# Kernel optimization log

Hardware: AMD Instinct MI355X
Metric: run time of the kernel (lower is better)

The kernel has to match this reference:

```python
import jax, jax.numpy as jnp
import numpy as np

B, C, H, W = 16, 256, 32, 32
DIM = H * W  # LayerNorm/Linear dim == h*w per the rearrange in forward


def _conv1x1(x, w, b):
    # x: [b,c,h,w], w: [out,in] (1x1 kernel squeezed), b: [out]
    return jnp.einsum('bchw,oc->bohw', x, w) + b[None, :, None, None]


def _layernorm(x, g, b, eps=1e-5):
    mu = jnp.mean(x, axis=-1, keepdims=True)
    var = jnp.var(x, axis=-1, keepdims=True)
    return (x - mu) / jnp.sqrt(var + eps) * g + b


def setup_inputs() -> dict:
    key = jax.random.key(0)
    ks = jax.random.split(key, 12)
    n = jax.random.normal
    k_cdc = (2.0 / (2 * C)) ** 0.5   # kaiming_normal fan_in = 2C
    k_v = (2.0 / C) ** 0.5           # fan_in = C
    k_lin = (2.0 / DIM) ** 0.5       # fan_in = DIM
    return {
        'x_spa': n(ks[0], (B, C, H, W), jnp.float32),
        'x_freq': n(ks[1], (B, C, H, W), jnp.float32),
        'w_cdc': n(ks[2], (C, 2 * C), jnp.float32) * k_cdc,
        'b_cdc': jnp.zeros((C,), jnp.float32),
        'w_sv': n(ks[3], (C, C), jnp.float32) * k_v,
        'b_sv': jnp.zeros((C,), jnp.float32),
        'w_fv': n(ks[4], (C, C), jnp.float32) * k_v,
        'b_fv': jnp.zeros((C,), jnp.float32),
        'ln_w': jnp.ones((DIM,), jnp.float32),
        'ln_b': jnp.zeros((DIM,), jnp.float32),
        'w_qk': n(ks[5], (2 * DIM, DIM), jnp.float32) * k_lin,  # Linear(dim, 2*dim), no bias
        'w_spa': n(ks[6], (DIM, DIM), jnp.float32) * k_lin,
        'b_spa': jnp.zeros((DIM,), jnp.float32),
        'w_frq': n(ks[7], (DIM, DIM), jnp.float32) * k_lin,
        'b_frq': jnp.zeros((DIM,), jnp.float32),
    }


def reference(x_spa, x_freq, w_cdc, b_cdc, w_sv, b_sv, w_fv, b_fv,
              ln_w, ln_b, w_qk, w_spa, b_spa, w_frq, b_frq):
    b, c, h, w = x_spa.shape
    hw = h * w
    scale = hw ** (-0.5)
    v_spa = _conv1x1(x_spa, w_sv, b_sv).reshape(b, c, hw)
    v_freq = _conv1x1(x_freq, w_fv, b_fv).reshape(b, c, hw)
    x = _conv1x1(jnp.concatenate([x_spa, x_freq], axis=1), w_cdc, b_cdc).reshape(b, c, hw)
    x = _layernorm(x, ln_w, ln_b)
    qk = x @ w_qk.T                       # [b, c, 2*hw]
    q, k = jnp.split(qk, 2, axis=-1)      # each [b, c, hw]
    att = jnp.einsum('bcn,bcm->bnm', q, k) * scale   # q^T k over channels: [b, hw, hw]
    att_spa = jax.nn.softmax(att @ w_spa.T + b_spa, axis=-1)
    att_frq = jax.nn.softmax(att @ w_frq.T + b_frq, axis=-1)
    out_spa = x_spa + jnp.einsum('bcn,bnm->bcm', v_spa, att_spa).reshape(b, c, h, w)
    out_freq = x_freq + jnp.einsum('bcn,bnm->bcm', v_freq, att_frq).reshape(b, c, h, w)
    return out_spa, out_freq
```

## Files before the change

kernel.cpp:

```cpp
#include <hip/hip_runtime.h>
#include <hip/hip_bf16.h>

typedef __hip_bfloat16 bf16;
typedef __attribute__((ext_vector_type(8))) short bf16x8v;
typedef __attribute__((ext_vector_type(4))) float f32x4v;

__device__ __forceinline__ float bfbits2f(unsigned short h) {
    union { unsigned int u; float f; } v; v.u = ((unsigned int)h) << 16; return v.f;
}
__device__ __forceinline__ unsigned short f2bfbits(float f) {
    bf16 h = __float2bfloat16(f);
    unsigned short s;
    __builtin_memcpy(&s, &h, 2);
    return s;
}
__device__ __forceinline__ float load1_any(const void* p, long idx, bool f32) {
    if (f32) return ((const float*)p)[idx];
    return bfbits2f(((const unsigned short*)p)[idx]);
}
__device__ __forceinline__ float4 loadbf4(const bf16* p) {
    ushort4 u = *reinterpret_cast<const ushort4*>(p);
    return make_float4(bfbits2f(u.x), bfbits2f(u.y), bfbits2f(u.z), bfbits2f(u.w));
}
__device__ __forceinline__ void store_bf4(bf16* p, float a, float b, float c, float d) {
    ushort4 o;
    o.x = f2bfbits(a); o.y = f2bfbits(b); o.z = f2bfbits(c); o.w = f2bfbits(d);
    *reinterpret_cast<ushort4*>(p) = o;
}
__device__ __forceinline__ void gl16(const void* g, void* l) {
    __builtin_amdgcn_global_load_lds(
        (const __attribute__((address_space(1))) unsigned int*)g,
        (__attribute__((address_space(3))) unsigned int*)l, 16, 0, 0);
}

__global__ __launch_bounds__(1024)
void detect_kernel(const unsigned short* __restrict__ x, int* __restrict__ flag) {
    const int tid = threadIdx.x;
    int zc = 0, hc = 0;
    const uint4* xv = (const uint4*)x;
#pragma unroll
    for (int p = 0; p < 16; ++p) {
        uint4 v = xv[p * 1024 + tid];
        unsigned s0 = v.x & 0xFFFFu, s1 = v.y & 0xFFFFu;
        unsigned s2 = v.z & 0xFFFFu, s3 = v.w & 0xFFFFu;
        zc += (int)(s0 == 0) + (int)(s1 == 0) + (int)(s2 == 0) + (int)(s3 == 0);
        hc += (int)(((s0 >> 7) & 0xFFu) >= 0x90u) + (int)(((s1 >> 7) & 0xFFu) >= 0x90u)
            + (int)(((s2 >> 7) & 0xFFu) >= 0x90u) + (int)(((s3 >> 7) & 0xFFu) >= 0x90u);
    }
#pragma unroll
    for (int off = 32; off > 0; off >>= 1) {
        zc += __shfl_down(zc, off);
        hc += __shfl_down(hc, off);
    }
    __shared__ int rz[16], rh[16];
    if ((tid & 63) == 0) { rz[tid >> 6] = zc; rh[tid >> 6] = hc; }
    __syncthreads();
    if (tid == 0) {
        int Z = 0, H = 0;
#pragma unroll
        for (int i = 0; i < 16; ++i) { Z += rz[i]; H += rh[i]; }
        flag[0] = (Z > 60000 || H > 256) ? 1 : 0;
        flag[1] = 1;
    }
}

__global__ void diag_kernel(float* __restrict__ out, float val) {
    if (threadIdx.x == 0) out[0] = val;
}

__global__ __launch_bounds__(256)
void convert6_kernel(const void* __restrict__ s0, const void* __restrict__ s1,
                     const void* __restrict__ s2, const void* __restrict__ s3,
                     const void* __restrict__ s4, const void* __restrict__ s5,
                     bf16* __restrict__ dst, const int* __restrict__ dflag) {
    const bool f32 = (*dflag != 0);
    for (long i = (long)blockIdx.x * 256 + threadIdx.x; i < 4456448;
         i += (long)gridDim.x * 256) {
        const void* s; long o;
        if (i < 131072)       { s = s0; o = i; }
        else if (i < 196608)  { s = s1; o = i - 131072; }
        else if (i < 262144)  { s = s2; o = i - 196608; }
        else if (i < 2359296) { s = s3; o = i - 262144; }
        else if (i < 3407872) { s = s4; o = i - 2359296; }
        else                  { s = s5; o = i - 3407872; }
        dst[i] = __float2bfloat16(load1_any(s, o, f32));
    }
}

__global__ __launch_bounds__(256)
void xpose_w_kernel(const bf16* __restrict__ src, bf16* __restrict__ dst) {
    __shared__ float t[64][65];
    const int c0 = blockIdx.x * 64, r0 = blockIdx.y * 64;
    const int tid = threadIdx.x;
#pragma unroll
    for (int p = 0; p < 16; ++p) {
        int e = tid + p * 256; int r = e >> 6, c = e & 63;
        t[r][c] = __bfloat162float(src[(long)(r0 + r) * 1024 + c0 + c]);
    }
    __syncthreads();
#pragma unroll
    for (int p = 0; p < 16; ++p) {
        int e = tid + p * 256; int r = e >> 6, c = e & 63;
        dst[(long)(c0 + r) * 1024 + r0 + c] = __float2bfloat16(t[c][r]);
    }
}

__global__ __launch_bounds__(256)
void build_wleft_kernel(const bf16* __restrict__ w_cdc, const bf16* __restrict__ w_sv,
                        const bf16* __restrict__ w_fv, bf16* __restrict__ W) {
    int i = blockIdx.x * 256 + threadIdx.x;
    if (i >= 393216) return;
    int r = i >> 9, c = i & 511;
    float v = 0.f;
    if (r < 256) v = __bfloat162float(w_cdc[r * 512 + c]);
    else if (r < 512) { if (c < 256) v = __bfloat162float(w_sv[(r - 256) * 256 + c]); }
    else              { if (c >= 256) v = __bfloat162float(w_fv[(r - 512) * 256 + (c - 256)]); }
    W[i] = __float2bfloat16(v);
}

__global__ __launch_bounds__(256)
void build_bcat_kernel(const void* __restrict__ b0, const void* __restrict__ b1,
                       const void* __restrict__ b2, float* __restrict__ bc,
                       const int* __restrict__ dflag) {
    const bool f32 = (*dflag != 0);
    int i = blockIdx.x * 256 + threadIdx.x;
    if (i < 256)      bc[i] = load1_any(b0, i, f32);
    else if (i < 512) bc[i] = load1_any(b1, i - 256, f32);
    else if (i < 768) bc[i] = load1_any(b2, i - 512, f32);
}

__global__ __launch_bounds__(256)
void xpose_conv_kernel(const void* __restrict__ x1, const void* __restrict__ x2,
                       bf16* __restrict__ dst, int bofs, int zsplit,
                       const int* __restrict__ dflag) {
    const bool f32 = (*dflag != 0);
    __shared__ float t[64][65];
    const int ch0 = blockIdx.y * 64, n0 = blockIdx.x * 64, z = blockIdx.z;
    const bool hiz = (z >= zsplit);
    const int zl = hiz ? z - zsplit : z;
    const void* x = hiz ? x2 : x1;
    const long sb = (long)(zl + bofs) * 262144, db = (long)z * 262144;
    const int tid = threadIdx.x;
#pragma unroll
    for (int p = 0; p < 16; ++p) {
        int e = tid + p * 256; int sch = e >> 6, sn = e & 63;
        t[sch][sn] = load1_any(x, sb + (long)(ch0 + sch) * 1024 + n0 + sn, f32);
    }
    __syncthreads();
#pragma unroll
    for (int p = 0; p < 16; ++p) {
        int e = tid + p * 256; int dn = e >> 6, dch = e & 63;
        dst[db + (long)(n0 + dn) * 256 + ch0 + dch] = __float2bfloat16(t[dch][dn]);
    }
}

__global__ __launch_bounds__(256)
void smnorm_kernel(bf16* __restrict__ X, float* __restrict__ invS) {
    const int tid = threadIdx.x;
    const int cg = tid & 7;
    const int js = tid >> 3;
    const int n0 = blockIdx.x * 64;
    const long zb = (long)blockIdx.y * 1048576;
    unsigned short* Xp = (unsigned short*)X + zb + n0 + cg * 8;

    float m[8];
#pragma unroll
    for (int q = 0; q < 8; ++q) m[q] = -3.4e38f;
#pragma unroll 4
    for (int r = 0; r < 32; ++r) {
        bf16x8v u = *(const bf16x8v*)(Xp + (long)(js * 32 + r) * 1024);
#pragma unroll
        for (int q = 0; q < 8; ++q)
            m[q] = fmaxf(m[q], bfbits2f((unsigned short)u[q]));
    }
    __shared__ float sh[32][8][8];
    __shared__ float Mc[64];
#pragma unroll
    for (int q = 0; q < 8; ++q) sh[js][cg][q] = m[q];
    __syncthreads();
    if (tid < 64) {
        float mm = -3.4e38f;
#pragma unroll 8
        for (int s = 0; s < 32; ++s) mm = fmaxf(mm, sh[s][tid >> 3][tid & 7]);
        Mc[tid] = mm;
    }
    __syncthreads();
    float M8[8], s8[8];
#pragma unroll
    for (int q = 0; q < 8; ++q) { M8[q] = Mc[cg * 8 + q]; s8[q] = 0.f; }
#pragma unroll 4
    for (int r = 0; r < 32; ++r) {
        long off = (long)(js * 32 + r) * 1024;
        bf16x8v u = *(const bf16x8v*)(Xp + off);
        bf16x8v o;
#pragma unroll
        for (int q = 0; q < 8; ++q) {
            float e = __expf(bfbits2f((unsigned short)u[q]) - M8[q]);
            s8[q] += e;
            o[q] = (short)f2bfbits(e);
        }
        *(bf16x8v*)(Xp + off) = o;
    }
    __syncthreads();
#pragma unroll
    for (int q = 0; q < 8; ++q) sh[js][cg][q] = s8[q];
    __syncthreads();
    if (tid < 64) {
        float ss = 0.f;
#pragma unroll 8
        for (int s = 0; s < 32; ++s) ss += sh[s][tid >> 3][tid & 7];
        invS[(long)blockIdx.y * 1024 + n0 + tid] = 1.0f / ss;
    }
}

__global__ __launch_bounds__(256)
void vscale_kernel(bf16* __restrict__ vb, const float* __restrict__ invS, int gN) {
    long base = ((long)blockIdx.x * 256 + threadIdx.x) * 8;
    if (base >= (long)512 * gN) return;
    int r = (int)(base / gN);
    long zn = base - (long)r * gN;
    const float* is = invS + (long)(r >> 8) * gN + zn;
    bf16x8v u = *(bf16x8v*)(vb + base);
    bf16x8v o;
#pragma unroll
    for (int q = 0; q < 8; ++q)
        o[q] = (short)f2bfbits(bfbits2f((unsigned short)u[q]) * is[q]);
    *(bf16x8v*)(vb + base) = o;
}

template <int MI, int EPI>
__global__ __launch_bounds__(256)
void mfma_nt(const bf16* __restrict__ A1, const bf16* __restrict__ A2,
             long aB1, long aB2, int ldA1, int ldA2,
             const bf16* __restrict__ B1, const bf16* __restrict__ B2,
             long bB1, long bB2, int ldB1, int ldB2,
             int ksplit, long kOff2,
             void* __restrict__ out1, void* __restrict__ out2,
             long oB1, long oB2, int ldO1, int ldO2,
             int K, float scale,
             const void* __restrict__ bias1, const void* __restrict__ bias2,
             const void* __restrict__ res1, const void* __restrict__ res2,
             long rBatch, int bofs, int zsplit,
             const int* __restrict__ dflag) {
    constexpr int BM = MI * 32;
    __shared__ short As[3][BM * 32];
    __shared__ short Bs[3][4096];
    const int tid  = threadIdx.x;
    const int lane = tid & 63, wave = tid >> 6;
    const int quad = lane >> 4, lrow = lane & 15;
    const int wm = (wave >> 1) * (MI * 16), wn = (wave & 1) * 64;

    int bx = blockIdx.x, by = blockIdx.y, bz = blockIdx.z;
    {
        const int gx = gridDim.x, gy = gridDim.y;
        const int gxy = gx * gy;
        const int ntot = gxy * gridDim.z;
        if ((ntot & 7) == 0) {
            int flat = bx + gx * (by + gy * bz);
            int w = (flat & 7) * (ntot >> 3) + (flat >> 3);
            bz = w / gxy;
            int rem = w - bz * gxy;
            by = rem / gx;
            bx = rem - by * gx;
        }
    }
    const int z  = bz;
    const bool hiz = (z >= zsplit);
    const int zl = hiz ? z - zsplit : z;
    const int n0 = bx * 128, m0 = by * BM;
    const int ldA = hiz ? ldA2 : ldA1, ldB = hiz ? ldB2 : ldB1;
    const int ldO = hiz ? ldO2 : ldO1;
    const int srow = tid >> 2, sseg = tid & 3;
    const int sl = sseg ^ ((srow >> 1) & 3);
    const int xq = quad ^ ((lrow >> 1) & 3);

    const bf16* Ab = (hiz ? A2 : A1) + (long)zl * (hiz ? aB2 : aB1);
    const bf16* Bb = (hiz ? B2 : B1) + (long)zl * (hiz ? bB2 : bB1);

    auto stage = [&](int buf, int k0) {
        const bf16* asrc = Ab + (long)k0;
        const bf16* bsrc = Bb + ((k0 < ksplit) ? (long)k0 : (long)(k0 - ksplit) + kOff2);
#pragma unroll
        for (int p = 0; p < MI / 2; ++p)
            gl16(asrc + (long)(m0 + p * 64 + srow) * ldA + sl * 8,
                 &As[buf][p * 2048 + wave * 512]);
        gl16(bsrc + (long)(n0 + srow) * ldB + sl * 8, &Bs[buf][wave * 512]);
        gl16(bsrc + (long)(n0 + 64 + srow) * ldB + sl * 8, &Bs[buf][2048 + wave * 512]);
    };

    f32x4v acc[MI][4] = {};
    const int nt = K >> 5;
    stage(0, 0);
    if (nt > 1) stage(1, 32);

    int cur = 0;
    for (int t = 0; t < nt; ++t) {
        if (t + 1 < nt) {
            if constexpr (MI == 4) asm volatile("s_waitcnt vmcnt(4)" ::: "memory");
            else                   asm volatile("s_waitcnt vmcnt(3)" ::: "memory");
        } else {
            asm volatile("s_waitcnt vmcnt(0)" ::: "memory");
        }
        __builtin_amdgcn_s_barrier();
        __builtin_amdgcn_sched_barrier(0);
        bf16x8v bfr[4], afr[MI];
#pragma unroll
        for (int j = 0; j < 4; ++j)
            bfr[j] = *(const bf16x8v*)&Bs[cur][(wn + j * 16 + lrow) * 32 + xq * 8];
#pragma unroll
        for (int i = 0; i < MI; ++i)
            afr[i] = *(const bf16x8v*)&As[cur][(wm + i * 16 + lrow) * 32 + xq * 8];
        asm volatile("s_waitcnt lgkmcnt(0)" ::: "memory");
        __builtin_amdgcn_sched_barrier(0);
        if (t + 2 < nt) {
            int nb = cur + 2; if (nb >= 3) nb -= 3;
            stage(nb, (t + 2) << 5);
        }
        __builtin_amdgcn_s_setprio(1);
#pragma unroll
        for (int i = 0; i < MI; ++i)
#pragma unroll
            for (int j = 0; j < 4; ++j)
                acc[i][j] = __builtin_amdgcn_mfma_f32_16x16x32_bf16(afr[i], bfr[j], acc[i][j], 0, 0, 0);
        __builtin_amdgcn_s_setprio(0);
        cur = (cur == 2) ? 0 : cur + 1;
    }

    const bool f32 = (*dflag != 0);
    const void* bias = hiz ? bias2 : bias1;
    if (EPI != 3) {
        bf16* O = (bf16*)(hiz ? out2 : out1) + (long)zl * (hiz ? oB2 : oB1);
#pragma unroll
        for (int i = 0; i < MI; ++i) {
            int row0 = m0 + wm + i * 16 + quad * 4;
            float rb[4] = {0.f, 0.f, 0.f, 0.f};
            if (EPI == 1 || EPI == 2) {
#pragma unroll
                for (int r = 0; r < 4; ++r) rb[r] = load1_any(bias, row0 + r, f32);
            }
#pragma unroll
            for (int j = 0; j < 4; ++j) {
                int col = n0 + wn + j * 16 + lrow;
#pragma unroll
                for (int r = 0; r < 4; ++r) {
                    float vv = acc[i][j][r];
                    if (EPI == 1) vv += rb[r];
                    if (EPI == 2) vv = vv * scale + rb[r];
                    O[(long)(row0 + r) * ldO + col] = __float2bfloat16(vv);
                }
            }
        }
    } else {
        float* O = (float*)(hiz ? out2 : out1);
        const void* res = hiz ? res2 : res1;
        const long ob  = (long)(zl + bofs) * (hiz ? oB2 : oB1);
        const long rbb = (long)(zl + bofs) * rBatch;
#pragma unroll
        for (int i = 0; i < MI; ++i) {
            int row0 = m0 + wm + i * 16 + quad * 4;
#pragma unroll
            for (int j = 0; j < 4; ++j) {
                int col = n0 + wn + j * 16 + lrow;
#pragma unroll
                for (int r = 0; r < 4; ++r) {
                    float rv = load1_any(res, rbb + (long)(row0 + r) * ldO + col, f32);
                    O[ob + (long)(row0 + r) * ldO + col] = acc[i][j][r] + rv;
                }
            }
        }
    }
}

__global__ __launch_bounds__(256)
void layernorm_kernel(const bf16* __restrict__ src, bf16* __restrict__ dst,
                      const void* __restrict__ g, const void* __restrict__ beta,
                      int gN, const int* __restrict__ dflag) {
    const bool f32 = (*dflag != 0);
    const int zc = blockIdx.x;
    const int zz = zc >> 8, c = zc & 255;
    const bf16* p = src + (long)c * gN + (long)zz * 1024;
    bf16* q = dst + (long)zc * 1024;
    const int tid = threadIdx.x;
    float4 v = loadbf4(p + tid * 4);
    float s  = v.x + v.y + v.z + v.w;
    float ss = v.x * v.x + v.y * v.y + v.z * v.z + v.w * v.w;
#pragma unroll
    for (int off = 32; off > 0; off >>= 1) {
        s  += __shfl_down(s, off);
        ss += __shfl_down(ss, off);
    }
    __shared__ float sh[8];
    __shared__ float sh_mu, sh_rs;
    if ((tid & 63) == 0) { sh[tid >> 6] = s; sh[4 + (tid >> 6)] = ss; }
    __syncthreads();
    if (tid == 0) {
        float S  = sh[0] + sh[1] + sh[2] + sh[3];
        float SS = sh[4] + sh[5] + sh[6] + sh[7];
        float mu = S * (1.0f / 1024.0f);
        float var = SS * (1.0f / 1024.0f) - mu * mu;
        sh_mu = mu;
        sh_rs = rsqrtf(fmaxf(var, 0.0f) + 1e-5f);
    }
    __syncthreads();
    float mu = sh_mu, rs = sh_rs;
    float gx = load1_any(g, tid * 4 + 0, f32), gy = load1_any(g, tid * 4 + 1, f32);
    float gz = load1_any(g, tid * 4 + 2, f32), gw = load1_any(g, tid * 4 + 3, f32);
    float bx = load1_any(beta, tid * 4 + 0, f32), by = load1_any(beta, tid * 4 + 1, f32);
    float bz = load1_any(beta, tid * 4 + 2, f32), bw = load1_any(beta, tid * 4 + 3, f32);
    store_bf4(q + tid * 4,
              (v.x - mu) * rs * gx + bx, (v.y - mu) * rs * gy + by,
              (v.z - mu) * rs * gz + bz, (v.w - mu) * rs * gw + bw);
}

extern "C" void kernel_launch(void* const* d_in, const int* in_sizes, int n_in,
                              void* d_out, int out_size, void* d_ws, size_t ws_size,
                              hipStream_t stream) {
    const void* x_spa  = d_in[0];
    const void* x_freq = d_in[1];
    const void* w_cdc  = d_in[2];
    const void* b_cdc  = d_in[3];
    const void* w_sv   = d_in[4];
    const void* b_sv   = d_in[5];
    const void* w_fv   = d_in[6];
    const void* b_fv   = d_in[7];
    const void* ln_w   = d_in[8];
    const void* ln_b   = d_in[9];
    const void* w_qk   = d_in[10];
    const void* w_spa  = d_in[11];
    const void* b_spa  = d_in[12];
    const void* w_frq  = d_in[13];
    const void* b_frq  = d_in[14];
    float* out = (float*)d_out;

    const int B = 16, C = 256;
    const long XB = 262144;
    const long PB = 1048576;

    int*   dflag = (int*)d_ws;
    float* bcat  = (float*)((char*)d_ws + 1024);
    bf16*  wb    = (bf16*)((char*)d_ws + 4096);
    bf16* w_cdc_b = wb;
    bf16* w_sv_b  = w_cdc_b + 131072;
    bf16* w_fv_b  = w_sv_b  + 65536;
    bf16* w_qk_b  = w_fv_b  + 65536;
    bf16* w_spa_b = w_qk_b  + 2097152;
    bf16* w_frq_b = w_spa_b + 1048576;
    bf16* w_qk_hiT= w_frq_b + 1048576;
    bf16* W1f     = w_qk_hiT + 1048576;
    bf16* Wleft   = W1f + 1048576;
    bf16* pb      = Wleft + 393216;

    const size_t fixedB = 4096 + 6946816ull * 2;
    const size_t perB   = 8921088ull;
    size_t avail = (ws_size > fixedB) ? (ws_size - fixedB) : 0;
    long gmax = (long)(avail / perB);
    const bool wsOK = (gmax >= 1);
    int G = wsOK ? (int)(gmax > 16 ? 16 : gmax) : 1;

    bf16* xT    = pb;
    bf16* XV    = xT  + 2L * G * XB;
    bf16* xln2  = XV  + 3L * G * XB;
    bf16* qTT   = xln2 + (long)G * XB;
    bf16* attpT = qTT + 3L * G * XB;
    float* invS = (float*)(attpT + 2L * G * PB);

    dim3 blk(256);
    detect_kernel<<<dim3(1), dim3(1024), 0, stream>>>((const unsigned short*)x_spa, dflag);

    if (!wsOK) {
        float mb = (float)(ws_size >> 20);
        diag_kernel<<<dim3(1), dim3(64), 0, stream>>>(out, 1000.0f * (mb + 1.0f));
        return;
    }

    convert6_kernel<<<dim3(4352), blk, 0, stream>>>(w_cdc, w_sv, w_fv, w_qk, w_spa, w_frq,
                                                    wb, dflag);
    xpose_w_kernel<<<dim3(16, 16), blk, 0, stream>>>(w_qk_b + 1048576, w_qk_hiT);
    build_wleft_kernel<<<dim3(1536), blk, 0, stream>>>(w_cdc_b, w_sv_b, w_fv_b, Wleft);
    build_bcat_kernel<<<dim3(3), blk, 0, stream>>>(b_cdc, b_sv, b_fv, bcat, dflag);
    mfma_nt<4, 0><<<dim3(8, 8, 2), blk, 0, stream>>>(
        w_spa_b, w_frq_b, 0, 0, 1024, 1024,
        w_qk_hiT, w_qk_hiT, 0, 0, 1024, 1024, 1024, 0,
        w_qk_b + 1048576, W1f, 0, 0, 1024, 1024,
        1024, 1.0f, nullptr, nullptr, nullptr, nullptr, 0, 0, 1, dflag);

    for (int b0 = 0; b0 < B; b0 += G) {
        int g = (B - b0 < G) ? (B - b0) : G;
        const int gN = g * 1024;
        bf16* vb = XV + 256L * gN;

        xpose_conv_kernel<<<dim3(16, 4, 2 * g), blk, 0, stream>>>(
            x_spa, x_freq, xT, b0, g, dflag);

        mfma_nt<4, 1><<<dim3(8 * g, 6, 1), blk, 0, stream>>>(
            Wleft, Wleft, 0, 0, 512, 512,
            xT, xT, 0, 0, 256, 256, 256, (long)g * XB,
            XV, XV, 0, 0, gN, gN,
            512, 1.0f, bcat, bcat, nullptr, nullptr, 0, 0, 1, dflag + 1);

        layernorm_kernel<<<dim3(g * C), blk, 0, stream>>>(XV, xln2, ln_w, ln_b, gN, dflag);

        mfma_nt<4, 0><<<dim3(2 * g, 8, 3), blk, 0, stream>>>(
            w_qk_b, W1f, 1048576, 0, 1024, 1024,
            xln2, xln2, 0, 0, 1024, 1024, 1024, 0,
            qTT, qTT + 2L * g * XB, (long)g * XB, 0, g * 256, g * 256,
            1024, 1.0f, nullptr, nullptr, nullptr, nullptr, 0, 0, 2, dflag);

        mfma_nt<4, 2><<<dim3(8, 8, 2 * g), blk, 0, stream>>>(
            qTT + (long)g * XB, qTT + 2L * g * XB, 256, 256, g * 256, g * 256,
            qTT, qTT, 256, 256, g * 256, g * 256, 256, 0,
            attpT, attpT + (long)g * PB, PB, PB, 1024, 1024,
            256, 0.03125f, b_spa, b_frq, nullptr, nullptr, 0, 0, g, dflag);

        smnorm_kernel<<<dim3(16, 2 * g), blk, 0, stream>>>(attpT, invS);

        vscale_kernel<<<dim3(gN / 4), blk, 0, stream>>>(vb, invS, gN);

        mfma_nt<2, 3><<<dim3(8, 4, 2 * g), blk, 0, stream>>>(
            vb, vb + 256L * gN, 1024, 1024, gN, gN,
            attpT, attpT + (long)g * PB, PB, PB, 1024, 1024, 1024, 0,
            out, out + 4194304, XB, XB, 1024, 1024,
            1024, 1.0f, nullptr, nullptr, x_spa, x_freq, XB, b0, g, dflag);
    }
}
```

Baseline: 348.7 us.

## Fuse V column scaling into softmax-norm kernel, reorder GEMM loop, retile final GEMM

Folds the per-column 1/sum scaling of V into the softmax normalization kernel, so the separate vscale launch and the global invS round trip go away. Each block scales its 64-column slice of V for its side and batch. In the GEMM main loop, the next-stage global prefetch is now issued before the LDS fragment loads, and the explicit lgkmcnt wait is removed so the loads can overlap. The final PV GEMM switches from MI=2 to MI=4 tiles with half as many blocks, trading parallelism for more reuse per block.

```diff
diff --git a/kernel.cpp b/kernel.cpp
--- a/kernel.cpp
+++ b/kernel.cpp
@@ -155,7 +155,7 @@
 }
 
 __global__ __launch_bounds__(256)
-void smnorm_kernel(bf16* __restrict__ X, float* __restrict__ invS) {
+void smnorm_kernel(bf16* __restrict__ X, bf16* __restrict__ vb, int gN, int gq) {
     const int tid = threadIdx.x;
     const int cg = tid & 7;
     const int js = tid >> 3;
@@ -175,6 +175,7 @@
     }
     __shared__ float sh[32][8][8];
     __shared__ float Mc[64];
+    __shared__ float Sc[64];
 #pragma unroll
     for (int q = 0; q < 8; ++q) sh[js][cg][q] = m[q];
     __syncthreads();
@@ -209,23 +210,25 @@
         float ss = 0.f;
 #pragma unroll 8
         for (int s = 0; s < 32; ++s) ss += sh[s][tid >> 3][tid & 7];
-        invS[(long)blockIdx.y * 1024 + n0 + tid] = 1.0f / ss;
-    }
-}
-
-__global__ __launch_bounds__(256)
-void vscale_kernel(bf16* __restrict__ vb, const float* __restrict__ invS, int gN) {
-    long base = ((long)blockIdx.x * 256 + threadIdx.x) * 8;
-    if (base >= (long)512 * gN) return;
-    int r = (int)(base / gN);
-    long zn = base - (long)r * gN;
-    const float* is = invS + (long)(r >> 8) * gN + zn;
-    bf16x8v u = *(bf16x8v*)(vb + base);
-    bf16x8v o;
-#pragma unroll
-    for (int q = 0; q < 8; ++q)
-        o[q] = (short)f2bfbits(bfbits2f((unsigned short)u[q]) * is[q]);
-    *(bf16x8v*)(vb + base) = o;
+        Sc[tid] = 1.0f / ss;
+    }
+    __syncthreads();
+    const int side = (blockIdx.y >= (unsigned)gq) ? 1 : 0;
+    const int zl = blockIdx.y - side * gq;
+    bf16* vp = vb + (long)(side * 256) * gN + (long)zl * 1024 + n0 + cg * 8;
+    float is8[8];
+#pragma unroll
+    for (int q = 0; q < 8; ++q) is8[q] = Sc[cg * 8 + q];
+#pragma unroll
+    for (int rr = 0; rr < 8; ++rr) {
+        long off = (long)(rr * 32 + js) * gN;
+        bf16x8v u = *(bf16x8v*)(vp + off);
+        bf16x8v o;
+#pragma unroll
+        for (int q = 0; q < 8; ++q)
+            o[q] = (short)f2bfbits(bfbits2f((unsigned short)u[q]) * is8[q]);
+        *(bf16x8v*)(vp + off) = o;
+    }
 }
 
 template <int MI, int EPI>
@@ -303,19 +306,17 @@
         }
         __builtin_amdgcn_s_barrier();
         __builtin_amdgcn_sched_barrier(0);
-        bf16x8v bfr[4], afr[MI];
-#pragma unroll
-        for (int j = 0; j < 4; ++j)
-            bfr[j] = *(const bf16x8v*)&Bs[cur][(wn + j * 16 + lrow) * 32 + xq * 8];
-#pragma unroll
-        for (int i = 0; i < MI; ++i)
-            afr[i] = *(const bf16x8v*)&As[cur][(wm + i * 16 + lrow) * 32 + xq * 8];
-        asm volatile("s_waitcnt lgkmcnt(0)" ::: "memory");
-        __builtin_amdgcn_sched_barrier(0);
         if (t + 2 < nt) {
             int nb = cur + 2; if (nb >= 3) nb -= 3;
             stage(nb, (t + 2) << 5);
         }
+        bf16x8v bfr[4], afr[MI];
+#pragma unroll
+        for (int j = 0; j < 4; ++j)
+            bfr[j] = *(const bf16x8v*)&Bs[cur][(wn + j * 16 + lrow) * 32 + xq * 8];
+#pragma unroll
+        for (int i = 0; i < MI; ++i)
+            afr[i] = *(const bf16x8v*)&As[cur][(wm + i * 16 + lrow) * 32 + xq * 8];
         __builtin_amdgcn_s_setprio(1);
 #pragma unroll
         for (int i = 0; i < MI; ++i)
@@ -462,7 +463,6 @@
     bf16* xln2  = XV  + 3L * G * XB;
     bf16* qTT   = xln2 + (long)G * XB;
     bf16* attpT = qTT + 3L * G * XB;
-    float* invS = (float*)(attpT + 2L * G * PB);
 
     dim3 blk(256);
     detect_kernel<<<dim3(1), dim3(1024), 0, stream>>>((const unsigned short*)x_spa, dflag);
@@ -512,11 +512,9 @@
             attpT, attpT + (long)g * PB, PB, PB, 1024, 1024,
             256, 0.03125f, b_spa, b_frq, nullptr, nullptr, 0, 0, g, dflag);
 
-        smnorm_kernel<<<dim3(16, 2 * g), blk, 0, stream>>>(attpT, invS);
-
-        vscale_kernel<<<dim3(gN / 4), blk, 0, stream>>>(vb, invS, gN);
-
-        mfma_nt<2, 3><<<dim3(8, 4, 2 * g), blk, 0, stream>>>(
+        smnorm_kernel<<<dim3(16, 2 * g), blk, 0, stream>>>(attpT, vb, gN, g);
+
+        mfma_nt<4, 3><<<dim3(8, 2, 2 * g), blk, 0, stream>>>(
             vb, vb + 256L * gN, 1024, 1024, gN, gN,
             attpT, attpT + (long)g * PB, PB, PB, 1024, 1024, 1024, 0,
             out, out + 4194304, XB, XB, 1024, 1024,
```

After: 349.2 us. About the same (+0.2%).
